# Kernel tuning notes

Hardware: AMD Instinct MI355X
Metric: run time of the kernel (lower is better)

The kernel has to match this reference:

```python
import jax, jax.numpy as jnp
import numpy as np

SEQ_LEN = 2048
DIM = 1024
K = 24
N_FFT = 4096  # nearest power of two >= 2*seq_len - 1


def setup_inputs() -> dict:
    key = jax.random.key(0)
    k1, k2, k3, k4 = jax.random.split(key, 4)
    x = jax.random.normal(k1, (4, SEQ_LEN, DIM), dtype=jnp.float32)
    filters = jax.random.normal(k2, (SEQ_LEN, K), dtype=jnp.float32) * 0.1
    M_inputs = jax.random.normal(k3, (DIM, DIM), dtype=jnp.float32) * (DIM ** -0.5)
    M_filters = jax.random.normal(k4, (K, DIM), dtype=jnp.float32) * (K ** -0.5)
    input_pos = jnp.arange(SEQ_LEN, dtype=jnp.int32)
    return {"x": x, "filters": filters, "M_inputs": M_inputs,
            "M_filters": M_filters, "input_pos": input_pos}


def reference(x, filters, M_inputs, M_filters, input_pos):
    # STU forward, use_approx=True, use_hankel_L=False, no flash_fft, no cache.
    B, S, D = x.shape
    # alternating sign +1,-1,+1,... along sequence
    sgn = jnp.where(jnp.arange(S) % 2 == 0, 1.0, -1.0).astype(x.dtype)[None, :, None]
    x_proj = x @ M_inputs                      # (B, S, D)
    phi_proj = filters @ M_filters             # (S, D)
    # v: (1, S, D, 1) -> rfft over seq axis with length N_FFT
    V = jnp.fft.rfft(phi_proj[None, :, :, None], n=N_FFT, axis=1)
    # U: stack [u, u*sgn] on last axis -> (B, S, D, 2)
    U = jnp.fft.rfft(jnp.stack([x_proj, x_proj * sgn], axis=-1), n=N_FFT, axis=1)
    U_conv = jnp.fft.irfft(V * U, n=N_FFT, axis=1)[:, :S]   # (B, S, D, 2)
    spectral_plus = U_conv[..., 0]
    spectral_minus = U_conv[..., 1] * sgn
    return spectral_plus + spectral_minus
```

## Files before the change

kernel.cpp:

```cpp
#include <hip/hip_runtime.h>
#include <hip/hip_bf16.h>
#include <stdint.h>
#include <stddef.h>

#define DIM 1024
#define SEQ 2048
#define KF 24

using f32x4    = __attribute__((ext_vector_type(4))) float;
using bf16x8   = __attribute__((ext_vector_type(8))) short;
using uint32x4 = __attribute__((ext_vector_type(4))) unsigned int;

__device__ __forceinline__ unsigned short f2bf(float f){
  union { float f; unsigned int i; } v; v.f = f;
  unsigned int r = v.i + 0x7FFFu + ((v.i >> 16) & 1u);
  return (unsigned short)(r >> 16);
}
__device__ __forceinline__ float dot2bf(unsigned int a, unsigned int b, float c){
  float d;
  asm("v_dot2_f32_bf16 %0, %1, %2, %3" : "=v"(d) : "v"(a), "v"(b), "v"(c));
  return d;
}
__device__ __forceinline__ unsigned vext(const uint32x4 v, int i){
  return i == 0 ? v.x : i == 1 ? v.y : i == 2 ? v.z : v.w;
}
__device__ __forceinline__ void gload_lds16(const void* g, void* l){
  __builtin_amdgcn_global_load_lds(
      (const __attribute__((address_space(1))) unsigned int*)g,
      (__attribute__((address_space(3))) unsigned int*)l, 16, 0, 0);
}
__device__ __forceinline__ uint32x4 make_srsrc(const void* base, unsigned bytes){
  uint32x4 r;
  r.x = (unsigned)(uintptr_t)base;
  r.y = (unsigned)((uintptr_t)base >> 32);
  r.z = bytes;
  r.w = 0x00020000u;
  return r;
}

__global__ void k_cvt_x(const float* __restrict__ x, unsigned short* __restrict__ xb){
  int i = blockIdx.x * 256 + threadIdx.x;
  const float4* x4 = (const float4*)x;
  float4 v = x4[i];
  ushort4 o;
  o.x = f2bf(v.x); o.y = f2bf(v.y); o.z = f2bf(v.z); o.w = f2bf(v.w);
  *(ushort4*)(xb + (size_t)i * 4) = o;
}

__global__ void k_tr_M(const float* __restrict__ Mi, unsigned short* __restrict__ MbT){
  __shared__ float tile[32][33];
  int e0 = blockIdx.y * 32, d0 = blockIdx.x * 32;
  int tx = threadIdx.x, ty = threadIdx.y;
  #pragma unroll
  for (int r = 0; r < 32; r += 8)
    tile[ty + r][tx] = Mi[(size_t)(e0 + ty + r) * DIM + d0 + tx];
  __syncthreads();
  #pragma unroll
  for (int r = 0; r < 32; r += 8)
    MbT[(size_t)(d0 + ty + r) * DIM + e0 + tx] = f2bf(tile[tx][ty + r]);
}

__global__ void k_pe(const float* __restrict__ filters, const float* __restrict__ Mf,
                     unsigned int* __restrict__ pepk2){
  int r2 = blockIdx.x * 256 + threadIdx.x;
  int d  = blockIdx.y;
  float a0 = 0.f, a1 = 0.f;
  #pragma unroll
  for (int k = 0; k < KF; ++k){
    float mf = Mf[(size_t)k * DIM + d];
    a0 += filters[(size_t)(4 * r2)     * KF + k] * mf;
    a1 += filters[(size_t)(4 * r2 + 2) * KF + k] * mf;
  }
  unsigned int lo = f2bf(2.f * a0), hi = f2bf(2.f * a1);
  pepk2[(size_t)(r2 >> 3) * 8192 + (size_t)d * 8 + (r2 & 7)] = lo | (hi << 16);
}

#define BM 128
#define BN 128
#define BKK 64
__global__ void k_gemm(const unsigned short* __restrict__ A,
                       const unsigned short* __restrict__ Bt,
                       unsigned int* __restrict__ Bg){
  __shared__ unsigned short As[BM * BKK];
  __shared__ unsigned short Bs[BN * BKK];
  int tid  = threadIdx.x;
  int lane = tid & 63, wave = tid >> 6;
  int wm = wave >> 1, wn = wave & 1;
  int trow0 = blockIdx.x * BM;
  int ncol0 = blockIdx.y * BN;

  f32x4 acc[4][4] = {};

  for (int kt = 0; kt < 1024 / BKK; ++kt){
    __syncthreads();
    #pragma unroll
    for (int g = 0; g < 4; ++g){
      int c  = wave * 4 + g;
      int mr = c * 8 + (lane >> 3);
      int u  = lane & 7;
      int su = u ^ (mr & 7);
      const unsigned short* srcA = A + (size_t)(trow0 + mr) * 1024 + kt * BKK + su * 8;
      gload_lds16(srcA, (char*)As + c * 1024);
      const unsigned short* srcB = Bt + (size_t)(ncol0 + mr) * 1024 + kt * BKK + su * 8;
      gload_lds16(srcB, (char*)Bs + c * 1024);
    }
    __syncthreads();

    bf16x8 af[4][2], bfr[4][2];
    #pragma unroll
    for (int mi = 0; mi < 4; ++mi){
      int row = wm * 64 + mi * 16 + (lane & 15);
      #pragma unroll
      for (int ks = 0; ks < 2; ++ks){
        int u = ((lane >> 4) + 4 * ks) ^ (row & 7);
        af[mi][ks] = *(const bf16x8*)((const char*)As + row * 128 + u * 16);
      }
    }
    #pragma unroll
    for (int ni = 0; ni < 4; ++ni){
      int row = wn * 64 + ni * 16 + (lane & 15);
      #pragma unroll
      for (int ks = 0; ks < 2; ++ks){
        int u = ((lane >> 4) + 4 * ks) ^ (row & 7);
        bfr[ni][ks] = *(const bf16x8*)((const char*)Bs + row * 128 + u * 16);
      }
    }
    #pragma unroll
    for (int mi = 0; mi < 4; ++mi)
      #pragma unroll
      for (int ni = 0; ni < 4; ++ni)
        #pragma unroll
        for (int ks = 0; ks < 2; ++ks)
          acc[mi][ni] = __builtin_amdgcn_mfma_f32_16x16x32_bf16(
              af[mi][ks], bfr[ni][ks], acc[mi][ni], 0, 0, 0);
  }

  unsigned short* Bh = (unsigned short*)Bg;
  #pragma unroll
  for (int mi = 0; mi < 4; ++mi)
    #pragma unroll
    for (int ni = 0; ni < 4; ++ni){
      int col = ncol0 + wn * 64 + ni * 16 + (lane & 15);
      #pragma unroll
      for (int reg = 0; reg < 4; ++reg){
        int row = trow0 + wm * 64 + mi * 16 + (lane >> 4) * 4 + reg;
        unsigned short y = f2bf(acc[mi][ni][reg]);
        int t = row & 2047, bq = row >> 11;
        int p = t & 1, j = t >> 1;
        size_t strm = ((size_t)bq * 2 + p) * 1048576;
        size_t e_lo = strm + (size_t)(j >> 2) * 4096 + (size_t)col * 4 + (j & 3);
        if (j == 0) Bg[e_lo] = (unsigned int)y;
        else        Bh[2 * e_lo] = y;
        if (j < 1023){
          int j1 = j + 1;
          size_t e_hi = strm + (size_t)(j1 >> 2) * 4096 + (size_t)col * 4 + (j1 & 3);
          Bh[2 * e_hi + 1] = y;
        }
      }
    }
}

#define BLX4(dst, so) \
  asm volatile("buffer_load_dwordx4 %0, %1, %2, %3 offen" \
               : "=v"(dst) : "v"(voff), "s"(xrsrc), "s"(so))
#define BLP4_0(dst, so) \
  asm volatile("buffer_load_dwordx4 %0, %1, %2, %3 offen" \
               : "=v"(dst) : "v"(pvoff), "s"(prsrc), "s"(so))
#define BLP4_16(dst, so) \
  asm volatile("buffer_load_dwordx4 %0, %1, %2, %3 offen offset:16" \
               : "=v"(dst) : "v"(pvoff), "s"(prsrc), "s"(so))

__device__ __forceinline__ void phase_old(const uint32x4* XBO, const uint32x4* pv,
                                          float* acc){
  #pragma unroll
  for (int q = 0; q < 8; ++q)
    #pragma unroll
    for (int m = 0; m < 32; ++m){
      int idx = m - 2 * q + 16;
      if (idx >= 2 && idx < 16)
        acc[m] = dot2bf(vext(pv[q >> 2], q & 3), vext(XBO[(idx >> 2) & 3], idx & 3),
                        acc[m]);
    }
}
__device__ __forceinline__ void phase_mid_new(const uint32x4* XBM, const uint32x4* XBN,
                                              const uint32x4* pv, float* acc){
  #pragma unroll
  for (int q = 0; q < 8; ++q)
    #pragma unroll
    for (int m = 0; m < 32; ++m){
      int idx = m - 2 * q + 16;
      if (idx >= 16){
        unsigned w = (idx < 32) ? vext(XBM[(idx >> 2) & 3], idx & 3)
                                : vext(XBN[(idx >> 2) & 3], idx & 3);
        acc[m] = dot2bf(vext(pv[q >> 2], q & 3), w, acc[m]);
      }
    }
}

#define BODY(XBO_, XBM_, XBN_, C) do{                                            \
  phase_old(XBO_, pv, acc);                                                      \
  __builtin_amdgcn_sched_barrier(0);                                             \
  { unsigned _xs = (unsigned)(4 * (C) + 4) * 16384u;                             \
    BLX4(XBO_[0], _xs);                                                          \
    BLX4(XBO_[1], _xs + 16384u);                                                 \
    BLX4(XBO_[2], _xs + 32768u);                                                 \
    BLX4(XBO_[3], _xs + 49152u);                                                 \
    unsigned _ps = pbase - 32768u * (unsigned)((C) + 1);                         \
    BLP4_0(npv[0], _ps); BLP4_16(npv[1], _ps); }                                 \
  __builtin_amdgcn_sched_barrier(0);                                             \
  phase_mid_new(XBM_, XBN_, pv, acc);                                            \
  asm volatile("s_waitcnt vmcnt(0)" ::: "memory");                               \
  __builtin_amdgcn_sched_barrier(0);                                             \
  pv[0] = npv[0]; pv[1] = npv[1];                                                \
}while(0)

__global__ __launch_bounds__(256, 4)
void k_conv(const unsigned int* __restrict__ Bg,
            const unsigned int* __restrict__ pepk2,
            float* __restrict__ out){
  int tid  = threadIdx.x;
  int bid  = blockIdx.x;
  int bp   = bid & 7;
  int rest = bid >> 3;
  int dblk = rest & 3;
  int mt   = 31 - (rest >> 2);
  int b = bp >> 1, p = bp & 1;
  int d = dblk * 256 + tid;

  uint32x4 xrsrc = make_srsrc(Bg + (size_t)bp * 1048576, 4194304u);
  uint32x4 prsrc = make_srsrc(pepk2, 2097152u);

  unsigned voff  = (unsigned)(d * 16);
  unsigned pvoff = (unsigned)(d * 32);

  uint32x4 B0[4], B1[4], B2[4], pv[2], npv[2];
  float acc[32];

  unsigned pbase = (2u * (unsigned)mt + 1u) * 32768u;
  int nch = 2 * mt + 2;

  #pragma unroll
  for (int m = 0; m < 32; ++m) acc[m] = 0.f;

  #pragma unroll
  for (int k = 0; k < 4; ++k) BLX4(B0[k], (unsigned)(k - 8) * 16384u);
  #pragma unroll
  for (int k = 0; k < 4; ++k) BLX4(B1[k], (unsigned)(k - 4) * 16384u);
  #pragma unroll
  for (int k = 0; k < 4; ++k) BLX4(B2[k], (unsigned)k * 16384u);
  BLP4_0(pv[0], pbase); BLP4_16(pv[1], pbase);
  asm volatile("s_waitcnt vmcnt(0)" ::: "memory");
  __builtin_amdgcn_sched_barrier(0);

  int c = 0;
  for (;;){
    BODY(B0, B1, B2, c); if (++c == nch) break;
    BODY(B1, B2, B0, c); if (++c == nch) break;
    BODY(B2, B0, B1, c); if (++c == nch) break;
  }

  float* oc = out + ((size_t)(b * SEQ + p) * 1024 + d) + (size_t)mt * 32 * 2048;
  #pragma unroll
  for (int m = 0; m < 32; ++m) oc[(size_t)m * 2048] = acc[m];
}

extern "C" void kernel_launch(void* const* d_in, const int* in_sizes, int n_in,
                              void* d_out, int out_size, void* d_ws, size_t ws_size,
                              hipStream_t stream){
  const float* x       = (const float*)d_in[0];
  const float* filters = (const float*)d_in[1];
  const float* Mi      = (const float*)d_in[2];
  const float* Mf      = (const float*)d_in[3];

  char* ws = (char*)d_ws;
  unsigned short* Xb    = (unsigned short*)(ws);
  unsigned int*   Bg    = (unsigned int*)  (ws + (size_t)16 * 1024 * 1024);
  unsigned short* MbT   = (unsigned short*)(ws + (size_t)48 * 1024 * 1024);
  unsigned int*   pepk2 = (unsigned int*)  (ws + (size_t)50 * 1024 * 1024);
  float* out = (float*)d_out;

  hipLaunchKernelGGL(k_cvt_x, dim3(8192), dim3(256), 0, stream, x, Xb);
  hipLaunchKernelGGL(k_tr_M,  dim3(32, 32), dim3(32, 8), 0, stream, Mi, MbT);
  hipLaunchKernelGGL(k_pe,    dim3(2, 1024), dim3(256), 0, stream, filters, Mf, pepk2);
  hipLaunchKernelGGL(k_gemm,  dim3(64, 8), dim3(256), 0, stream, Xb, MbT, Bg);
  hipLaunchKernelGGL(k_conv,  dim3(1024), dim3(256), 65536, stream, Bg, pepk2, out);
}
```

Measured before the change: 128.9 us.

## Compute two adjacent output tiles per conv block to share X register loads

Each k_conv block now accumulates two consecutive 32-row output tiles (A and B), each with its own filter vectors and accumulators. Both tiles reuse the same rotating X buffers, so X loads per output roughly halve. The grid drops from 1024 to 512 blocks and the unused 64 KB dynamic LDS request is removed. The cost is about 32 more accumulator registers, occupancy lowered to 3 waves per SIMD, fewer blocks to spread the triangular workload, and tile A reading filter offsets past its valid range in the last chunks, which relies on out-of-bounds buffer loads returning zero.

Measured after the change: 154.7 us. 20.1% more time.

```diff
diff --git a/kernel.cpp b/kernel.cpp
--- a/kernel.cpp
+++ b/kernel.cpp
@@ -197,24 +197,29 @@
     }
 }
 
-#define BODY(XBO_, XBM_, XBN_, C) do{                                            \
-  phase_old(XBO_, pv, acc);                                                      \
+#define BODY2(XBO_, XBM_, XBN_, C) do{                                           \
+  phase_old(XBO_, pvA, accA);                                                    \
+  phase_old(XBO_, pvB, accB);                                                    \
   __builtin_amdgcn_sched_barrier(0);                                             \
   { unsigned _xs = (unsigned)(4 * (C) + 4) * 16384u;                             \
     BLX4(XBO_[0], _xs);                                                          \
     BLX4(XBO_[1], _xs + 16384u);                                                 \
     BLX4(XBO_[2], _xs + 32768u);                                                 \
     BLX4(XBO_[3], _xs + 49152u);                                                 \
-    unsigned _ps = pbase - 32768u * (unsigned)((C) + 1);                         \
-    BLP4_0(npv[0], _ps); BLP4_16(npv[1], _ps); }                                 \
+    unsigned _psA = pbaseA - 32768u * (unsigned)((C) + 1);                       \
+    unsigned _psB = pbaseB - 32768u * (unsigned)((C) + 1);                       \
+    BLP4_0(npvA[0], _psA); BLP4_16(npvA[1], _psA);                               \
+    BLP4_0(npvB[0], _psB); BLP4_16(npvB[1], _psB); }                             \
   __builtin_amdgcn_sched_barrier(0);                                             \
-  phase_mid_new(XBM_, XBN_, pv, acc);                                            \
+  phase_mid_new(XBM_, XBN_, pvA, accA);                                          \
+  phase_mid_new(XBM_, XBN_, pvB, accB);                                          \
   asm volatile("s_waitcnt vmcnt(0)" ::: "memory");                               \
   __builtin_amdgcn_sched_barrier(0);                                             \
-  pv[0] = npv[0]; pv[1] = npv[1];                                                \
+  pvA[0] = npvA[0]; pvA[1] = npvA[1];                                            \
+  pvB[0] = npvB[0]; pvB[1] = npvB[1];                                            \
 }while(0)
 
-__global__ __launch_bounds__(256, 4)
+__global__ __launch_bounds__(256, 3)
 void k_conv(const unsigned int* __restrict__ Bg,
             const unsigned int* __restrict__ pepk2,
             float* __restrict__ out){
@@ -223,7 +228,8 @@
   int bp   = bid & 7;
   int rest = bid >> 3;
   int dblk = rest & 3;
-  int mt   = 31 - (rest >> 2);
+  int pk   = 15 - (rest >> 2);
+  int mt   = 2 * pk;
   int b = bp >> 1, p = bp & 1;
   int d = dblk * 256 + tid;
 
@@ -233,14 +239,16 @@
   unsigned voff  = (unsigned)(d * 16);
   unsigned pvoff = (unsigned)(d * 32);
 
-  uint32x4 B0[4], B1[4], B2[4], pv[2], npv[2];
-  float acc[32];
-
-  unsigned pbase = (2u * (unsigned)mt + 1u) * 32768u;
-  int nch = 2 * mt + 2;
-
-  #pragma unroll
-  for (int m = 0; m < 32; ++m) acc[m] = 0.f;
+  uint32x4 B0[4], B1[4], B2[4];
+  uint32x4 pvA[2], npvA[2], pvB[2], npvB[2];
+  float accA[32], accB[32];
+
+  unsigned pbaseA = (2u * (unsigned)mt + 1u) * 32768u;
+  unsigned pbaseB = (2u * (unsigned)mt + 3u) * 32768u;
+  int nch = 2 * mt + 4;
+
+  #pragma unroll
+  for (int m = 0; m < 32; ++m){ accA[m] = 0.f; accB[m] = 0.f; }
 
   #pragma unroll
   for (int k = 0; k < 4; ++k) BLX4(B0[k], (unsigned)(k - 8) * 16384u);
@@ -248,20 +256,24 @@
   for (int k = 0; k < 4; ++k) BLX4(B1[k], (unsigned)(k - 4) * 16384u);
   #pragma unroll
   for (int k = 0; k < 4; ++k) BLX4(B2[k], (unsigned)k * 16384u);
-  BLP4_0(pv[0], pbase); BLP4_16(pv[1], pbase);
+  BLP4_0(pvA[0], pbaseA); BLP4_16(pvA[1], pbaseA);
+  BLP4_0(pvB[0], pbaseB); BLP4_16(pvB[1], pbaseB);
   asm volatile("s_waitcnt vmcnt(0)" ::: "memory");
   __builtin_amdgcn_sched_barrier(0);
 
   int c = 0;
   for (;;){
-    BODY(B0, B1, B2, c); if (++c == nch) break;
-    BODY(B1, B2, B0, c); if (++c == nch) break;
-    BODY(B2, B0, B1, c); if (++c == nch) break;
+    BODY2(B0, B1, B2, c); if (++c == nch) break;
+    BODY2(B1, B2, B0, c); if (++c == nch) break;
+    BODY2(B2, B0, B1, c); if (++c == nch) break;
   }
 
-  float* oc = out + ((size_t)(b * SEQ + p) * 1024 + d) + (size_t)mt * 32 * 2048;
-  #pragma unroll
-  for (int m = 0; m < 32; ++m) oc[(size_t)m * 2048] = acc[m];
+  float* ocA = out + ((size_t)(b * SEQ + p) * 1024 + d) + (size_t)mt * 32 * 2048;
+  float* ocB = ocA + (size_t)32 * 2048;
+  #pragma unroll
+  for (int m = 0; m < 32; ++m) ocA[(size_t)m * 2048] = accA[m];
+  #pragma unroll
+  for (int m = 0; m < 32; ++m) ocB[(size_t)m * 2048] = accB[m];
 }
 
 extern "C" void kernel_launch(void* const* d_in, const int* in_sizes, int n_in,
@@ -283,5 +295,5 @@
   hipLaunchKernelGGL(k_tr_M,  dim3(32, 32), dim3(32, 8), 0, stream, Mi, MbT);
   hipLaunchKernelGGL(k_pe,    dim3(2, 1024), dim3(256), 0, stream, filters, Mf, pepk2);
   hipLaunchKernelGGL(k_gemm,  dim3(64, 8), dim3(256), 0, stream, Xb, MbT, Bg);
-  hipLaunchKernelGGL(k_conv,  dim3(1024), dim3(256), 65536, stream, Bg, pepk2, out);
-}
+  hipLaunchKernelGGL(k_conv,  dim3(512), dim3(256), 0, stream, Bg, pepk2, out);
+}
```
